# Kernel optimization log

Measured on AMD Instinct MI355X. Metric: run time of the kernel, lower is better.

The kernel has to match this reference:

```python
import jax, jax.numpy as jnp
import numpy as np

N = 50000
E = 1600000
IN_DIM = 64
EMB_DIM = 64
DENSE = 128
HEADS = 2
GATD = 64
SLOPE = 0.2


def gat_conv(x, src, dst, W, al, ar, b):
    # DGL GATConv: x [N, Fin], W [Fin, H*D], al/ar/b [H, D]
    n = x.shape[0]
    H, D = al.shape
    z = (x @ W).reshape(n, H, D)                      # [N,H,D]
    el = jnp.sum(z * al, axis=-1)                     # [N,H]
    er = jnp.sum(z * ar, axis=-1)                     # [N,H]
    e = jax.nn.leaky_relu(el[src] + er[dst], SLOPE)   # [E,H]
    # edge softmax grouped by destination node
    m = jax.ops.segment_max(e, dst, num_segments=n)   # [N,H]
    ex = jnp.exp(e - m[dst])                          # [E,H]
    s = jax.ops.segment_sum(ex, dst, num_segments=n)  # [N,H]
    alpha = ex / s[dst]                               # [E,H]
    out = jax.ops.segment_sum(alpha[:, :, None] * z[src], dst, num_segments=n)
    return out + b                                    # [N,H,D]


def setup_inputs() -> dict:
    key = jax.random.key(0)
    ks = jax.random.split(key, 20)
    g = lambda k, sh: jax.random.normal(k, sh, dtype=jnp.float32) * 0.05
    inp = {
        "feat": jax.random.normal(ks[0], (N, IN_DIM), dtype=jnp.float32),
        "node_ids": jax.random.randint(ks[1], (N,), 0, N, dtype=jnp.int32),
        "src": jax.random.randint(ks[2], (E,), 0, N, dtype=jnp.int32),
        "dst": jax.random.randint(ks[3], (E,), 0, N, dtype=jnp.int32),
        "emb": g(ks[4], (N, EMB_DIM)),
        "dense_w": g(ks[5], (IN_DIM + EMB_DIM, DENSE)),
        "dense_b": jnp.zeros((DENSE,), jnp.float32),
        "g1_w": g(ks[6], (DENSE, HEADS * GATD)),
        "g1_al": g(ks[7], (HEADS, GATD)),
        "g1_ar": g(ks[8], (HEADS, GATD)),
        "g1_b": jnp.zeros((HEADS, GATD), jnp.float32),
        "g2_w": g(ks[9], (HEADS * GATD, HEADS * GATD)),
        "g2_al": g(ks[10], (HEADS, GATD)),
        "g2_ar": g(ks[11], (HEADS, GATD)),
        "g2_b": jnp.zeros((HEADS, GATD), jnp.float32),
        "out_w": g(ks[12], (HEADS * GATD, 1)),
        "out_al": g(ks[13], (1, 1)),
        "out_ar": g(ks[14], (1, 1)),
        "out_b": jnp.zeros((1, 1), jnp.float32),
    }
    return inp


def reference(feat, node_ids, src, dst, emb, dense_w, dense_b,
              g1_w, g1_al, g1_ar, g1_b, g2_w, g2_al, g2_ar, g2_b,
              out_w, out_al, out_ar, out_b):
    # embedding concat + initial dense + ReLU
    h = jnp.concatenate([emb[node_ids], feat], axis=-1)   # [N, 128]
    h = jax.nn.relu(h @ dense_w + dense_b)                # [N, 128]
    # GAT layer 1: ReLU then concat heads (reshape N, H*D)
    h = jax.nn.relu(gat_conv(h, src, dst, g1_w, g1_al, g1_ar, g1_b))
    h = h.reshape(h.shape[0], -1)                         # [N, H*D]
    # GAT layer 2
    h = jax.nn.relu(gat_conv(h, src, dst, g2_w, g2_al, g2_ar, g2_b))
    h = h.reshape(h.shape[0], -1)
    # output GAT layer, 1 head, squeeze head dim
    h = gat_conv(h, src, dst, out_w, out_al, out_ar, out_b)  # [N,1,1]
    return h[:, 0, :]                                        # [N,1]
```

## Files before the change

### kernel.cpp

```cpp
#include <hip/hip_runtime.h>
#include <cfloat>
#include <cmath>


#define CBG 256
#define CAPC 12288
#define TILE 4096
#define BIMG 10240

typedef __attribute__((ext_vector_type(8))) short short8v;
typedef __attribute__((ext_vector_type(4))) float f32x4;

__device__ __forceinline__ float lrelu(float x) { return x > 0.f ? x : 0.2f * x; }

__device__ __forceinline__ uint32_t bf16_rne(float f) {
  uint32_t u = __float_as_uint(f);
  return (u + 0x7fffu + ((u >> 16) & 1u)) >> 16;
}
__device__ __forceinline__ uint32_t pack_hilo(float v) {
  uint32_t h = bf16_rne(v);
  float r = v - __uint_as_float(h << 16);
  return (h << 16) | bf16_rne(r);
}

__global__ __launch_bounds__(256) void bucketA_kernel(
    const int* __restrict__ src, const int* __restrict__ dst,
    int* __restrict__ scount, uint32_t* __restrict__ tmp, int e, int ncb) {
  __shared__ int cnt[256];
  __shared__ int lscan[256];
  __shared__ int gbase[256];
  __shared__ uint32_t image[TILE];
  const int t = threadIdx.x;
  const int e0 = blockIdx.x * TILE;
  const int ne = min(TILE, e - e0);

  for (int i = t; i < 256; i += 256) cnt[i] = 0;
  __syncthreads();
  for (int i = t; i < ne; i += 256) atomicAdd(&cnt[dst[e0 + i] >> 8], 1);
  __syncthreads();
  if (t < 64) {
    int carry = 0;
    for (int base = 0; base < ncb; base += 64) {
      int idx = base + t;
      int c = (idx < ncb) ? cnt[idx] : 0;
      int v = c;
#pragma unroll
      for (int off = 1; off < 64; off <<= 1) {
        int u = __shfl_up(v, off, 64);
        if (t >= off) v += u;
      }
      if (idx < ncb) lscan[idx] = carry + v - c;
      carry += __shfl(v, 63, 64);
    }
  }
  __syncthreads();
  for (int b = t; b < ncb; b += 256)
    gbase[b] = (cnt[b] > 0) ? atomicAdd(&scount[b], cnt[b]) : 0;
  __syncthreads();
  for (int b = t; b < ncb; b += 256) cnt[b] = 0;
  __syncthreads();
  for (int i = t; i < ne; i += 256) {
    int d = dst[e0 + i], s = src[e0 + i];
    int b = d >> 8;
    int r = atomicAdd(&cnt[b], 1);
    image[lscan[b] + r] =
        (uint32_t)s | ((uint32_t)(d & 255) << 16) | ((uint32_t)b << 24);
  }
  __syncthreads();
  for (int j = t; j < ne; j += 256) {
    uint32_t w = image[j];
    int b = w >> 24;
    int pos = gbase[b] + (j - lscan[b]);
    if (pos < CAPC) tmp[(size_t)b * CAPC + pos] = w & 0xFFFFFFu;
  }
}

__global__ __launch_bounds__(256) void bucketB_kernel(
    const uint32_t* __restrict__ tmp, const int* __restrict__ scount,
    int* __restrict__ row_start, int* __restrict__ csr_src, int n, int ncb, int e) {
  __shared__ int cnt[256];
  __shared__ int cur[256];
  __shared__ int wsum[4];
  __shared__ int s_base;
  __shared__ uint32_t image[BIMG];
  const int b = blockIdx.x, t = threadIdx.x, lane = t & 63, wid = t >> 6;

  if (t < 64) {
    int part = 0;
    for (int idx = lane; idx < b; idx += 64) part += scount[idx];
#pragma unroll
    for (int off = 32; off; off >>= 1) part += __shfl_xor(part, off, 64);
    if (lane == 0) s_base = part;
  }
  cnt[t] = 0;
  __syncthreads();
  const int total = min(scount[b], CAPC);
  const int base = s_base;
  const uint32_t* strm = tmp + (size_t)b * CAPC;

  for (int i = t; i < total; i += 256) atomicAdd(&cnt[(strm[i] >> 16) & 255], 1);
  __syncthreads();
  int c = cnt[t], v = c;
#pragma unroll
  for (int off = 1; off < 64; off <<= 1) {
    int u = __shfl_up(v, off, 64);
    if (lane >= off) v += u;
  }
  if (lane == 63) wsum[wid] = v;
  __syncthreads();
  if (t == 0) {
    int acc = 0;
#pragma unroll
    for (int w = 0; w < 4; w++) { int x = wsum[w]; wsum[w] = acc; acc += x; }
  }
  __syncthreads();
  int ex = wsum[wid] + v - c;
  cur[t] = ex;
  int d = b * CBG + t;
  if (d < n) row_start[d] = base + ex;
  if (b == 0 && t == 0) row_start[n] = e;
  __syncthreads();
  for (int i = t; i < total; i += 256) {
    uint32_t w = strm[i];
    int dl = (w >> 16) & 255;
    int pos = atomicAdd(&cur[dl], 1);
    if (pos < BIMG) image[pos] = w & 0xFFFFu;
    else csr_src[base + pos] = (int)(w & 0xFFFFu);
  }
  __syncthreads();
  const int lim = total < BIMG ? total : BIMG;
  for (int j = t; j < lim; j += 256) csr_src[base + j] = (int)image[j];
}

__global__ void hist_kernel(const int* __restrict__ dst, int* __restrict__ cnt, int e) {
  for (int i = blockIdx.x * blockDim.x + threadIdx.x; i < e; i += gridDim.x * blockDim.x)
    atomicAdd(&cnt[dst[i]], 1);
}
__global__ void scatter_kernel(const int* __restrict__ src, const int* __restrict__ dst,
                               const int* __restrict__ row_start, int* __restrict__ cursor,
                               int* __restrict__ csr_src, int e) {
  for (int i = blockIdx.x * blockDim.x + threadIdx.x; i < e; i += gridDim.x * blockDim.x) {
    int d = dst[i];
    int pos = atomicAdd(&cursor[d], 1);
    csr_src[row_start[d] + pos] = src[i];
  }
}
__global__ __launch_bounds__(1024) void scan1_kernel(const int* __restrict__ cnt,
                                                     int* __restrict__ row_start,
                                                     int* __restrict__ bsum, int n) {
  __shared__ int wsum[16];
  const int t = threadIdx.x, lane = t & 63, wid = t >> 6;
  int i = blockIdx.x * 1024 + t;
  int c = (i < n) ? cnt[i] : 0;
  int v = c;
#pragma unroll
  for (int off = 1; off < 64; off <<= 1) {
    int u = __shfl_up(v, off, 64);
    if (lane >= off) v += u;
  }
  if (lane == 63) wsum[wid] = v;
  __syncthreads();
  if (t == 0) {
    int acc = 0;
#pragma unroll
    for (int w = 0; w < 16; w++) { int x = wsum[w]; wsum[w] = acc; acc += x; }
    bsum[blockIdx.x] = acc;
  }
  __syncthreads();
  if (i < n) row_start[i] = wsum[wid] + v - c;
}
__global__ __launch_bounds__(64) void scan2_kernel(int* __restrict__ bsum, int nb) {
  const int lane = threadIdx.x;
  int carry = 0;
  for (int base = 0; base < nb; base += 64) {
    int idx = base + lane;
    int c = (idx < nb) ? bsum[idx] : 0;
    int v = c;
#pragma unroll
    for (int off = 1; off < 64; off <<= 1) {
      int u = __shfl_up(v, off, 64);
      if (lane >= off) v += u;
    }
    if (idx < nb) bsum[idx] = carry + v - c;
    carry += __shfl(v, 63, 64);
  }
}
__global__ void scan3_kernel(int* __restrict__ row_start, const int* __restrict__ bsum,
                             int n, int e) {
  int i = blockIdx.x * blockDim.x + threadIdx.x;
  if (i < n) row_start[i] += bsum[i >> 10];
  if (i == 0) row_start[n] = e;
}

__global__ __launch_bounds__(256) void wswz3_kernel(
    const float* __restrict__ W0, const float* __restrict__ W1,
    const float* __restrict__ W2, short* __restrict__ Whi0,
    short* __restrict__ Wlo0, short* __restrict__ Whi1, short* __restrict__ Wlo1,
    short* __restrict__ Whi2, short* __restrict__ Wlo2) {
  int which = blockIdx.x >> 3;
  const float* W = which == 0 ? W0 : (which == 1 ? W1 : W2);
  short* Whi = which == 0 ? Whi0 : (which == 1 ? Whi1 : Whi2);
  short* Wlo = which == 0 ? Wlo0 : (which == 1 ? Wlo1 : Wlo2);
  int fid = (blockIdx.x & 7) * 256 + threadIdx.x;
  int lane = fid & 63;
  int cq = fid >> 6;
  int q = cq >> 3, c = cq & 7;
  int col = c * 16 + (lane & 15);
  int k0 = q * 32 + (lane >> 4) * 8;
#pragma unroll
  for (int j = 0; j < 8; j++) {
    float v = W[(k0 + j) * 128 + col];
    uint32_t h = bf16_rne(v);
    float r = v - __uint_as_float(h << 16);
    Whi[fid * 8 + j] = (short)h;
    Wlo[fid * 8 + j] = (short)bf16_rne(r);
  }
}

template <int MODE>
__global__ __launch_bounds__(256) void mfmm_kernel(
    const uint32_t* __restrict__ Xp, const short* __restrict__ Whi,
    const short* __restrict__ Wlo, const float* __restrict__ bias,
    uint32_t* __restrict__ Hp, uint32_t* __restrict__ zp,
    float2* __restrict__ el2, float2* __restrict__ er2,
    const float* __restrict__ al, const float* __restrict__ ar, int n,
    const float* __restrict__ emb, const int* __restrict__ ids,
    const float* __restrict__ feat) {
  __shared__ short Ahi[64 * 136];
  __shared__ short Alo[64 * 136];
  const int t = threadIdx.x;
  const int nb = blockIdx.x * 64;

  for (int idx = t; idx < 64 * 32; idx += 256) {
    int nl = idx >> 5, k4 = (idx & 31) << 2;
    int node = nb + nl;
    uint32_t h01 = 0, h23 = 0, l01 = 0, l23 = 0;
    if (node < n) {
      if (MODE == 1) {
        uint4 w = *(const uint4*)&Xp[(size_t)node * 128 + k4];
        h01 = (w.x >> 16) | (w.y & 0xffff0000u);
        l01 = (w.x & 0xffffu) | (w.y << 16);
        h23 = (w.z >> 16) | (w.w & 0xffff0000u);
        l23 = (w.z & 0xffffu) | (w.w << 16);
      } else {
        float4 v;
        if (k4 < 64) v = *(const float4*)&emb[(size_t)ids[node] * 64 + k4];
        else         v = *(const float4*)&feat[(size_t)node * 64 + (k4 - 64)];
        uint32_t a0 = bf16_rne(v.x), a1 = bf16_rne(v.y);
        uint32_t a2 = bf16_rne(v.z), a3 = bf16_rne(v.w);
        h01 = a0 | (a1 << 16);
        h23 = a2 | (a3 << 16);
        l01 = bf16_rne(v.x - __uint_as_float(a0 << 16)) |
              (bf16_rne(v.y - __uint_as_float(a1 << 16)) << 16);
        l23 = bf16_rne(v.z - __uint_as_float(a2 << 16)) |
              (bf16_rne(v.w - __uint_as_float(a3 << 16)) << 16);
      }
    }
    *(uint2*)&Ahi[nl * 136 + k4] = make_uint2(h01, h23);
    *(uint2*)&Alo[nl * 136 + k4] = make_uint2(l01, l23);
  }
  __syncthreads();

  const int lane = t & 63, wv = t >> 6;
  const int r16 = lane & 15, g = lane >> 4;
  const int arow = (wv * 16 + r16) * 136;

  f32x4 acc[8];
#pragma unroll
  for (int c = 0; c < 8; c++) acc[c] = (f32x4){0.f, 0.f, 0.f, 0.f};

#pragma unroll
  for (int q = 0; q < 4; q++) {
    int ka = q * 32 + g * 8;
    short8v ahi = *(const short8v*)&Ahi[arow + ka];
    short8v alo = *(const short8v*)&Alo[arow + ka];
#pragma unroll
    for (int c = 0; c < 8; c++) {
      short8v bhi = *(const short8v*)&Whi[(((q * 8 + c) * 64) + lane) * 8];
      short8v blo = *(const short8v*)&Wlo[(((q * 8 + c) * 64) + lane) * 8];
      acc[c] = __builtin_amdgcn_mfma_f32_16x16x32_bf16(ahi, bhi, acc[c], 0, 0, 0);
      acc[c] = __builtin_amdgcn_mfma_f32_16x16x32_bf16(ahi, blo, acc[c], 0, 0, 0);
      acc[c] = __builtin_amdgcn_mfma_f32_16x16x32_bf16(alo, bhi, acc[c], 0, 0, 0);
    }
  }

  const int node_base = nb + wv * 16;
  if (MODE == 0) {
#pragma unroll
    for (int c = 0; c < 8; c++) {
      int col = c * 16 + r16;
      float bv = bias[col];
#pragma unroll
      for (int r = 0; r < 4; r++) {
        int node = node_base + g * 4 + r;
        if (node < n) {
          float v = fmaxf(acc[c][r] + bv, 0.f);
          Hp[(size_t)node * 128 + col] = pack_hilo(v);
        }
      }
    }
  } else {
    float p0l[4] = {0, 0, 0, 0}, p1l[4] = {0, 0, 0, 0};
    float p0r[4] = {0, 0, 0, 0}, p1r[4] = {0, 0, 0, 0};
#pragma unroll
    for (int c = 0; c < 8; c++) {
      int col = c * 16 + r16;
      float av = al[col], rv = ar[col];
#pragma unroll
      for (int r = 0; r < 4; r++) {
        if (c < 4) { p0l[r] = fmaf(acc[c][r], av, p0l[r]); p0r[r] = fmaf(acc[c][r], rv, p0r[r]); }
        else       { p1l[r] = fmaf(acc[c][r], av, p1l[r]); p1r[r] = fmaf(acc[c][r], rv, p1r[r]); }
      }
    }
#pragma unroll
    for (int c = 0; c < 8; c++) {
#pragma unroll
      for (int r = 0; r < 4; r++) {
        float other = __shfl_xor(acc[c][r], 1, 64);
        int node = node_base + g * 4 + r;
        if (!(lane & 1) && node < n) {
          uint32_t w = bf16_rne(acc[c][r]) | (bf16_rne(other) << 16);
          zp[(size_t)node * 64 + c * 8 + (r16 >> 1)] = w;
        }
      }
    }
#pragma unroll
    for (int off = 1; off < 16; off <<= 1) {
#pragma unroll
      for (int r = 0; r < 4; r++) {
        p0l[r] += __shfl_xor(p0l[r], off, 64);
        p1l[r] += __shfl_xor(p1l[r], off, 64);
        p0r[r] += __shfl_xor(p0r[r], off, 64);
        p1r[r] += __shfl_xor(p1r[r], off, 64);
      }
    }
    if (r16 == 0) {
#pragma unroll
      for (int r = 0; r < 4; r++) {
        int node = node_base + g * 4 + r;
        if (node < n) {
          el2[node] = make_float2(p0l[r], p1l[r]);
          er2[node] = make_float2(p0r[r], p1r[r]);
        }
      }
    }
  }
}

#define CAP 256
__global__ __launch_bounds__(256) void agg12_kernel(
    const uint32_t* __restrict__ zp, const float2* __restrict__ el2,
    const float2* __restrict__ er2, const int* __restrict__ row_start,
    const int* __restrict__ csr_src, const float* __restrict__ bias,
    uint32_t* __restrict__ Hp,
    const float* __restrict__ ow, const float* __restrict__ oal,
    const float* __restrict__ oar, float* __restrict__ z3,
    float* __restrict__ el3, float* __restrict__ er3, int n, int fuse_out) {
  __shared__ float2 ec[4][CAP];
  __shared__ int sc[4][CAP];
  const int w = threadIdx.x >> 6, lane = threadIdx.x & 63;
  const int node = blockIdx.x * 4 + w;
  const bool valid = node < n;
  int rs = 0, deg = 0;
  float er0 = 0.f, er1 = 0.f;
  if (valid) {
    rs = row_start[node];
    deg = row_start[node + 1] - rs;
    float2 e2 = er2[node];
    er0 = e2.x; er1 = e2.y;
  }
  const int cdeg = deg < CAP ? deg : CAP;

  float sp0 = 0.f, sp1 = 0.f;
  for (int i = lane; i < deg; i += 64) {
    int s = csr_src[rs + i];
    float2 l = el2[s];
    float x0 = __expf(lrelu(l.x + er0));
    float x1 = __expf(lrelu(l.y + er1));
    if (i < CAP) { sc[w][i] = s; ec[w][i] = make_float2(x0, x1); }
    sp0 += x0; sp1 += x1;
  }
#pragma unroll
  for (int off = 32; off; off >>= 1) {
    sp0 += __shfl_xor(sp0, off, 64);
    sp1 += __shfl_xor(sp1, off, 64);
  }
  __syncthreads();

  float ae = 0.f, ao = 0.f;
  int i = 0;
  for (; i + 8 <= cdeg; i += 8) {
    uint32_t zw[8];
    float xh[8];
#pragma unroll
    for (int u = 0; u < 8; u++) {
      int s = sc[w][i + u];
      float2 ex = ec[w][i + u];
      xh[u] = (lane < 32) ? ex.x : ex.y;
      zw[u] = zp[(size_t)s * 64 + lane];
    }
#pragma unroll
    for (int u = 0; u < 8; u++) {
      ae = fmaf(xh[u], __uint_as_float(zw[u] << 16), ae);
      ao = fmaf(xh[u], __uint_as_float(zw[u] & 0xffff0000u), ao);
    }
  }
  for (; i < cdeg; i++) {
    int s = sc[w][i];
    float2 ex = ec[w][i];
    float x = (lane < 32) ? ex.x : ex.y;
    uint32_t zw = zp[(size_t)s * 64 + lane];
    ae = fmaf(x, __uint_as_float(zw << 16), ae);
    ao = fmaf(x, __uint_as_float(zw & 0xffff0000u), ao);
  }
  for (; i < deg; i++) {
    int s = csr_src[rs + i];
    float2 l = el2[s];
    float x0 = __expf(lrelu(l.x + er0));
    float x1 = __expf(lrelu(l.y + er1));
    float x = (lane < 32) ? x0 : x1;
    uint32_t zw = zp[(size_t)s * 64 + lane];
    ae = fmaf(x, __uint_as_float(zw << 16), ae);
    ao = fmaf(x, __uint_as_float(zw & 0xffff0000u), ao);
  }

  if (valid) {
    float sp = (lane < 32) ? sp0 : sp1;
    float2 b2 = reinterpret_cast<const float2*>(bias)[lane];
    float oe, oo;
    if (deg == 0) { oe = b2.x; oo = b2.y; }
    else { oe = ae / sp + b2.x; oo = ao / sp + b2.y; }
    oe = fmaxf(oe, 0.f);
    oo = fmaxf(oo, 0.f);
    if (!fuse_out) {
      *(uint2*)&Hp[(size_t)node * 128 + 2 * lane] =
          make_uint2(pack_hilo(oe), pack_hilo(oo));
    } else {
      float2 w2 = reinterpret_cast<const float2*>(ow)[lane];
      float d = oe * w2.x + oo * w2.y;
#pragma unroll
      for (int off = 32; off; off >>= 1) d += __shfl_xor(d, off, 64);
      if (lane == 0) {
        z3[node] = d;
        el3[node] = d * oal[0];
        er3[node] = d * oar[0];
      }
    }
  }
}

__global__ __launch_bounds__(256) void agg3_kernel(
    const float* __restrict__ z3, const float* __restrict__ el3,
    const float* __restrict__ er3, const int* __restrict__ row_start,
    const int* __restrict__ csr_src, const float* __restrict__ b,
    float* __restrict__ out, int n) {
  int node = blockIdx.x * 8 + (threadIdx.x >> 5);
  int l32 = threadIdx.x & 31;
  if (node >= n) return;
  int rs = row_start[node];
  int deg = row_start[node + 1] - rs;
  float er = er3[node];
  float sp = 0.f, ap = 0.f;
  for (int i = l32; i < deg; i += 32) {
    int s = csr_src[rs + i];
    float ex = __expf(lrelu(el3[s] + er));
    sp += ex;
    ap = fmaf(ex, z3[s], ap);
  }
#pragma unroll
  for (int off = 16; off; off >>= 1) {
    sp += __shfl_xor(sp, off, 64);
    ap += __shfl_xor(ap, off, 64);
  }
  if (l32 == 0) out[node] = (deg == 0) ? b[0] : (ap / sp + b[0]);
}

extern "C" void kernel_launch(void* const* d_in, const int* in_sizes, int n_in,
                              void* d_out, int out_size, void* d_ws, size_t ws_size,
                              hipStream_t stream) {
  const float* feat     = (const float*)d_in[0];
  const int*   node_ids = (const int*)d_in[1];
  const int*   src      = (const int*)d_in[2];
  const int*   dst      = (const int*)d_in[3];
  const float* emb      = (const float*)d_in[4];
  const float* dense_w  = (const float*)d_in[5];
  const float* dense_b  = (const float*)d_in[6];
  const float* g1_w     = (const float*)d_in[7];
  const float* g1_al    = (const float*)d_in[8];
  const float* g1_ar    = (const float*)d_in[9];
  const float* g1_b     = (const float*)d_in[10];
  const float* g2_w     = (const float*)d_in[11];
  const float* g2_al    = (const float*)d_in[12];
  const float* g2_ar    = (const float*)d_in[13];
  const float* g2_b     = (const float*)d_in[14];
  const float* out_w    = (const float*)d_in[15];
  const float* out_al   = (const float*)d_in[16];
  const float* out_ar   = (const float*)d_in[17];
  const float* out_b    = (const float*)d_in[18];
  const int n = in_sizes[0] / 64;
  const int e = in_sizes[2];

  const int ncb = (n + CBG - 1) / CBG;

  char* ws = (char*)d_ws;
  size_t off = 0;
  auto alloc = [&](size_t bytes) -> void* {
    void* p = ws + off;
    off += (bytes + 255) & ~(size_t)255;
    return p;
  };
  uint32_t* Hp       = (uint32_t*)alloc((size_t)n * 128 * 4);
  size_t zp_bytes    = (size_t)n * 64 * 4;
  size_t tmp_bytes   = (size_t)ncb * CAPC * 4;
  uint32_t* zp       = (uint32_t*)alloc(zp_bytes > tmp_bytes ? zp_bytes : tmp_bytes);
  uint32_t* tmp      = zp;
  float2*   el2      = (float2*)alloc((size_t)n * 8);
  float2*   er2      = (float2*)alloc((size_t)n * 8);
  float*    z3       = (float*)alloc((size_t)n * 4);
  float*    el3      = (float*)alloc((size_t)n * 4);
  float*    er3      = (float*)alloc((size_t)n * 4);
  int*      scount   = (int*)alloc((size_t)ncb * 4);
  int*      row_start= (int*)alloc((size_t)(n + 1) * 4);
  int*      csr_src  = (int*)alloc((size_t)e * 4);
  short*    Wd_hi    = (short*)alloc(2048 * 8 * 2);
  short*    Wd_lo    = (short*)alloc(2048 * 8 * 2);
  short*    W1_hi    = (short*)alloc(2048 * 8 * 2);
  short*    W1_lo    = (short*)alloc(2048 * 8 * 2);
  short*    W2_hi    = (short*)alloc(2048 * 8 * 2);
  short*    W2_lo    = (short*)alloc(2048 * 8 * 2);
  int*      cnt      = (int*)alloc((size_t)n * 4);
  int*      cursor   = (int*)alloc((size_t)n * 4);
  const int nblk     = (n + 1023) / 1024;
  int*      bsum     = (int*)alloc((size_t)nblk * 4);

  wswz3_kernel<<<24, 256, 0, stream>>>(dense_w, g1_w, g2_w,
                                       Wd_hi, Wd_lo, W1_hi, W1_lo, W2_hi, W2_lo);

  if (n < 65536) {
    hipMemsetAsync(scount, 0, (size_t)ncb * 4, stream);
    const int natile = (e + TILE - 1) / TILE;
    bucketA_kernel<<<natile, 256, 0, stream>>>(src, dst, scount, tmp, e, ncb);
    bucketB_kernel<<<ncb, 256, 0, stream>>>(tmp, scount, row_start, csr_src,
                                            n, ncb, e);
  } else {
    hipMemsetAsync(cnt, 0, (size_t)n * 4, stream);
    hipMemsetAsync(cursor, 0, (size_t)n * 4, stream);
    hist_kernel<<<2048, 256, 0, stream>>>(dst, cnt, e);
    scan1_kernel<<<nblk, 1024, 0, stream>>>(cnt, row_start, bsum, n);
    scan2_kernel<<<1, 64, 0, stream>>>(bsum, nblk);
    scan3_kernel<<<(n + 255) / 256, 256, 0, stream>>>(row_start, bsum, n, e);
    scatter_kernel<<<2048, 256, 0, stream>>>(src, dst, row_start, cursor, csr_src, e);
  }

  const int mmgrid = (n + 63) / 64;
  const int ngrid4 = (n + 3) / 4;
  const int ngrid8 = (n + 7) / 8;

  mfmm_kernel<0><<<mmgrid, 256, 0, stream>>>(nullptr, Wd_hi, Wd_lo, dense_b,
                                             Hp, nullptr, nullptr, nullptr,
                                             nullptr, nullptr, n, emb, node_ids, feat);
  mfmm_kernel<1><<<mmgrid, 256, 0, stream>>>(Hp, W1_hi, W1_lo, nullptr,
                                             nullptr, zp, el2, er2,
                                             g1_al, g1_ar, n, nullptr, nullptr, nullptr);
  agg12_kernel<<<ngrid4, 256, 0, stream>>>(zp, el2, er2, row_start, csr_src, g1_b, Hp,
                                           nullptr, nullptr, nullptr, nullptr, nullptr,
                                           nullptr, n, 0);
  mfmm_kernel<1><<<mmgrid, 256, 0, stream>>>(Hp, W2_hi, W2_lo, nullptr,
                                             nullptr, zp, el2, er2,
                                             g2_al, g2_ar, n, nullptr, nullptr, nullptr);
  agg12_kernel<<<ngrid4, 256, 0, stream>>>(zp, el2, er2, row_start, csr_src, g2_b, nullptr,
                                           out_w, out_al, out_ar, z3, el3, er3, n, 1);
  agg3_kernel<<<ngrid8, 256, 0, stream>>>(z3, el3, er3, row_start, csr_src, out_b,
                                          (float*)d_out, n);
}
```

Before: 240.3 us.

## Fuse CSR bucket pass with dense layer; fold memset into weight prep

Replaces the scount memset with an extra block in the weight-swizzle kernel, and merges bucketB with the first dense matmul into one launch whose blocks split by index. The two stages are independent, so they can run concurrently and the launch count drops. Bucket tile size is halved to give bucketA more blocks. The shared memory buffer is now sized for the larger of the two bodies, which may lower occupancy for the matmul blocks.

```diff
diff --git a/kernel.cpp b/kernel.cpp
--- a/kernel.cpp
+++ b/kernel.cpp
@@ -5,7 +5,7 @@
 
 #define CBG 256
 #define CAPC 12288
-#define TILE 4096
+#define TILE 2048
 #define BIMG 10240
 
 typedef __attribute__((ext_vector_type(8))) short short8v;
@@ -21,6 +21,36 @@
   uint32_t h = bf16_rne(v);
   float r = v - __uint_as_float(h << 16);
   return (h << 16) | bf16_rne(r);
+}
+
+__global__ __launch_bounds__(256) void prep_kernel(
+    const float* __restrict__ W0, const float* __restrict__ W1,
+    const float* __restrict__ W2, short* __restrict__ Whi0,
+    short* __restrict__ Wlo0, short* __restrict__ Whi1, short* __restrict__ Wlo1,
+    short* __restrict__ Whi2, short* __restrict__ Wlo2,
+    int* __restrict__ scount, int ncb) {
+  if (blockIdx.x >= 24) {
+    for (int i = threadIdx.x; i < ncb; i += 256) scount[i] = 0;
+    return;
+  }
+  int which = blockIdx.x >> 3;
+  const float* W = which == 0 ? W0 : (which == 1 ? W1 : W2);
+  short* Whi = which == 0 ? Whi0 : (which == 1 ? Whi1 : Whi2);
+  short* Wlo = which == 0 ? Wlo0 : (which == 1 ? Wlo1 : Wlo2);
+  int fid = (blockIdx.x & 7) * 256 + threadIdx.x;
+  int lane = fid & 63;
+  int cq = fid >> 6;
+  int q = cq >> 3, c = cq & 7;
+  int col = c * 16 + (lane & 15);
+  int k0 = q * 32 + (lane >> 4) * 8;
+#pragma unroll
+  for (int j = 0; j < 8; j++) {
+    float v = W[(k0 + j) * 128 + col];
+    uint32_t h = bf16_rne(v);
+    float r = v - __uint_as_float(h << 16);
+    Whi[fid * 8 + j] = (short)h;
+    Wlo[fid * 8 + j] = (short)bf16_rne(r);
+  }
 }
 
 __global__ __launch_bounds__(256) void bucketA_kernel(
@@ -75,27 +105,28 @@
   }
 }
 
-__global__ __launch_bounds__(256) void bucketB_kernel(
-    const uint32_t* __restrict__ tmp, const int* __restrict__ scount,
-    int* __restrict__ row_start, int* __restrict__ csr_src, int n, int ncb, int e) {
-  __shared__ int cnt[256];
-  __shared__ int cur[256];
-  __shared__ int wsum[4];
-  __shared__ int s_base;
-  __shared__ uint32_t image[BIMG];
-  const int b = blockIdx.x, t = threadIdx.x, lane = t & 63, wid = t >> 6;
+__device__ __forceinline__ void bucketB_body(
+    int b, char* smem, const uint32_t* __restrict__ tmp,
+    const int* __restrict__ scount, int* __restrict__ row_start,
+    int* __restrict__ csr_src, int n, int ncb, int e) {
+  int* cnt = (int*)smem;
+  int* cur = cnt + 256;
+  int* wsum = cur + 256;
+  int* s_base = wsum + 4;
+  uint32_t* image = (uint32_t*)(smem + 2080);
+  const int t = threadIdx.x, lane = t & 63, wid = t >> 6;
 
   if (t < 64) {
     int part = 0;
     for (int idx = lane; idx < b; idx += 64) part += scount[idx];
 #pragma unroll
     for (int off = 32; off; off >>= 1) part += __shfl_xor(part, off, 64);
-    if (lane == 0) s_base = part;
+    if (lane == 0) *s_base = part;
   }
   cnt[t] = 0;
   __syncthreads();
   const int total = min(scount[b], CAPC);
-  const int base = s_base;
+  const int base = *s_base;
   const uint32_t* strm = tmp + (size_t)b * CAPC;
 
   for (int i = t; i < total; i += 256) atomicAdd(&cnt[(strm[i] >> 16) & 255], 1);
@@ -132,93 +163,9 @@
   for (int j = t; j < lim; j += 256) csr_src[base + j] = (int)image[j];
 }
 
-__global__ void hist_kernel(const int* __restrict__ dst, int* __restrict__ cnt, int e) {
-  for (int i = blockIdx.x * blockDim.x + threadIdx.x; i < e; i += gridDim.x * blockDim.x)
-    atomicAdd(&cnt[dst[i]], 1);
-}
-__global__ void scatter_kernel(const int* __restrict__ src, const int* __restrict__ dst,
-                               const int* __restrict__ row_start, int* __restrict__ cursor,
-                               int* __restrict__ csr_src, int e) {
-  for (int i = blockIdx.x * blockDim.x + threadIdx.x; i < e; i += gridDim.x * blockDim.x) {
-    int d = dst[i];
-    int pos = atomicAdd(&cursor[d], 1);
-    csr_src[row_start[d] + pos] = src[i];
-  }
-}
-__global__ __launch_bounds__(1024) void scan1_kernel(const int* __restrict__ cnt,
-                                                     int* __restrict__ row_start,
-                                                     int* __restrict__ bsum, int n) {
-  __shared__ int wsum[16];
-  const int t = threadIdx.x, lane = t & 63, wid = t >> 6;
-  int i = blockIdx.x * 1024 + t;
-  int c = (i < n) ? cnt[i] : 0;
-  int v = c;
-#pragma unroll
-  for (int off = 1; off < 64; off <<= 1) {
-    int u = __shfl_up(v, off, 64);
-    if (lane >= off) v += u;
-  }
-  if (lane == 63) wsum[wid] = v;
-  __syncthreads();
-  if (t == 0) {
-    int acc = 0;
-#pragma unroll
-    for (int w = 0; w < 16; w++) { int x = wsum[w]; wsum[w] = acc; acc += x; }
-    bsum[blockIdx.x] = acc;
-  }
-  __syncthreads();
-  if (i < n) row_start[i] = wsum[wid] + v - c;
-}
-__global__ __launch_bounds__(64) void scan2_kernel(int* __restrict__ bsum, int nb) {
-  const int lane = threadIdx.x;
-  int carry = 0;
-  for (int base = 0; base < nb; base += 64) {
-    int idx = base + lane;
-    int c = (idx < nb) ? bsum[idx] : 0;
-    int v = c;
-#pragma unroll
-    for (int off = 1; off < 64; off <<= 1) {
-      int u = __shfl_up(v, off, 64);
-      if (lane >= off) v += u;
-    }
-    if (idx < nb) bsum[idx] = carry + v - c;
-    carry += __shfl(v, 63, 64);
-  }
-}
-__global__ void scan3_kernel(int* __restrict__ row_start, const int* __restrict__ bsum,
-                             int n, int e) {
-  int i = blockIdx.x * blockDim.x + threadIdx.x;
-  if (i < n) row_start[i] += bsum[i >> 10];
-  if (i == 0) row_start[n] = e;
-}
-
-__global__ __launch_bounds__(256) void wswz3_kernel(
-    const float* __restrict__ W0, const float* __restrict__ W1,
-    const float* __restrict__ W2, short* __restrict__ Whi0,
-    short* __restrict__ Wlo0, short* __restrict__ Whi1, short* __restrict__ Wlo1,
-    short* __restrict__ Whi2, short* __restrict__ Wlo2) {
-  int which = blockIdx.x >> 3;
-  const float* W = which == 0 ? W0 : (which == 1 ? W1 : W2);
-  short* Whi = which == 0 ? Whi0 : (which == 1 ? Whi1 : Whi2);
-  short* Wlo = which == 0 ? Wlo0 : (which == 1 ? Wlo1 : Wlo2);
-  int fid = (blockIdx.x & 7) * 256 + threadIdx.x;
-  int lane = fid & 63;
-  int cq = fid >> 6;
-  int q = cq >> 3, c = cq & 7;
-  int col = c * 16 + (lane & 15);
-  int k0 = q * 32 + (lane >> 4) * 8;
-#pragma unroll
-  for (int j = 0; j < 8; j++) {
-    float v = W[(k0 + j) * 128 + col];
-    uint32_t h = bf16_rne(v);
-    float r = v - __uint_as_float(h << 16);
-    Whi[fid * 8 + j] = (short)h;
-    Wlo[fid * 8 + j] = (short)bf16_rne(r);
-  }
-}
-
 template <int MODE>
-__global__ __launch_bounds__(256) void mfmm_kernel(
+__device__ __forceinline__ void mfmm_body(
+    int bid, char* smem,
     const uint32_t* __restrict__ Xp, const short* __restrict__ Whi,
     const short* __restrict__ Wlo, const float* __restrict__ bias,
     uint32_t* __restrict__ Hp, uint32_t* __restrict__ zp,
@@ -226,10 +173,10 @@
     const float* __restrict__ al, const float* __restrict__ ar, int n,
     const float* __restrict__ emb, const int* __restrict__ ids,
     const float* __restrict__ feat) {
-  __shared__ short Ahi[64 * 136];
-  __shared__ short Alo[64 * 136];
+  short* Ahi = (short*)smem;
+  short* Alo = Ahi + 64 * 136;
   const int t = threadIdx.x;
-  const int nb = blockIdx.x * 64;
+  const int nb = bid * 64;
 
   for (int idx = t; idx < 64 * 32; idx += 256) {
     int nl = idx >> 5, k4 = (idx & 31) << 2;
@@ -345,6 +292,92 @@
       }
     }
   }
+}
+
+__global__ __launch_bounds__(256) void mfmm0_bktB_kernel(
+    const uint32_t* __restrict__ tmp, const int* __restrict__ scount,
+    int* __restrict__ row_start, int* __restrict__ csr_src, int ncbB,
+    const short* __restrict__ Whi, const short* __restrict__ Wlo,
+    const float* __restrict__ bias, uint32_t* __restrict__ Hp, int n, int ncb,
+    int e, const float* __restrict__ emb, const int* __restrict__ ids,
+    const float* __restrict__ feat) {
+  __shared__ __align__(16) char smem[43040];
+  if ((int)blockIdx.x < ncbB) {
+    bucketB_body(blockIdx.x, smem, tmp, scount, row_start, csr_src, n, ncb, e);
+  } else {
+    mfmm_body<0>(blockIdx.x - ncbB, smem, nullptr, Whi, Wlo, bias, Hp,
+                 nullptr, nullptr, nullptr, nullptr, nullptr, n, emb, ids, feat);
+  }
+}
+
+__global__ __launch_bounds__(256) void mfmm1_kernel(
+    const uint32_t* __restrict__ Xp, const short* __restrict__ Whi,
+    const short* __restrict__ Wlo, uint32_t* __restrict__ zp,
+    float2* __restrict__ el2, float2* __restrict__ er2,
+    const float* __restrict__ al, const float* __restrict__ ar, int n) {
+  __shared__ __align__(16) char smem[64 * 136 * 2 * 2];
+  mfmm_body<1>(blockIdx.x, smem, Xp, Whi, Wlo, nullptr, nullptr, zp, el2, er2,
+               al, ar, n, nullptr, nullptr, nullptr);
+}
+
+__global__ void hist_kernel(const int* __restrict__ dst, int* __restrict__ cnt, int e) {
+  for (int i = blockIdx.x * blockDim.x + threadIdx.x; i < e; i += gridDim.x * blockDim.x)
+    atomicAdd(&cnt[dst[i]], 1);
+}
+__global__ void scatter_kernel(const int* __restrict__ src, const int* __restrict__ dst,
+                               const int* __restrict__ row_start, int* __restrict__ cursor,
+                               int* __restrict__ csr_src, int e) {
+  for (int i = blockIdx.x * blockDim.x + threadIdx.x; i < e; i += gridDim.x * blockDim.x) {
+    int d = dst[i];
+    int pos = atomicAdd(&cursor[d], 1);
+    csr_src[row_start[d] + pos] = src[i];
+  }
+}
+__global__ __launch_bounds__(1024) void scan1_kernel(const int* __restrict__ cnt,
+                                                     int* __restrict__ row_start,
+                                                     int* __restrict__ bsum, int n) {
+  __shared__ int wsum[16];
+  const int t = threadIdx.x, lane = t & 63, wid = t >> 6;
+  int i = blockIdx.x * 1024 + t;
+  int c = (i < n) ? cnt[i] : 0;
+  int v = c;
+#pragma unroll
+  for (int off = 1; off < 64; off <<= 1) {
+    int u = __shfl_up(v, off, 64);
+    if (lane >= off) v += u;
+  }
+  if (lane == 63) wsum[wid] = v;
+  __syncthreads();
+  if (t == 0) {
+    int acc = 0;
+#pragma unroll
+    for (int w = 0; w < 16; w++) { int x = wsum[w]; wsum[w] = acc; acc += x; }
+    bsum[blockIdx.x] = acc;
+  }
+  __syncthreads();
+  if (i < n) row_start[i] = wsum[wid] + v - c;
+}
+__global__ __launch_bounds__(64) void scan2_kernel(int* __restrict__ bsum, int nb) {
+  const int lane = threadIdx.x;
+  int carry = 0;
+  for (int base = 0; base < nb; base += 64) {
+    int idx = base + lane;
+    int c = (idx < nb) ? bsum[idx] : 0;
+    int v = c;
+#pragma unroll
+    for (int off = 1; off < 64; off <<= 1) {
+      int u = __shfl_up(v, off, 64);
+      if (lane >= off) v += u;
+    }
+    if (idx < nb) bsum[idx] = carry + v - c;
+    carry += __shfl(v, 63, 64);
+  }
+}
+__global__ void scan3_kernel(int* __restrict__ row_start, const int* __restrict__ bsum,
+                             int n, int e) {
+  int i = blockIdx.x * blockDim.x + threadIdx.x;
+  if (i < n) row_start[i] += bsum[i >> 10];
+  if (i == 0) row_start[n] = e;
 }
 
 #define CAP 256
@@ -533,15 +566,20 @@
   const int nblk     = (n + 1023) / 1024;
   int*      bsum     = (int*)alloc((size_t)nblk * 4);
 
-  wswz3_kernel<<<24, 256, 0, stream>>>(dense_w, g1_w, g2_w,
-                                       Wd_hi, Wd_lo, W1_hi, W1_lo, W2_hi, W2_lo);
+  const int mmgrid = (n + 63) / 64;
+  const int ngrid4 = (n + 3) / 4;
+  const int ngrid8 = (n + 7) / 8;
+
+  prep_kernel<<<25, 256, 0, stream>>>(dense_w, g1_w, g2_w,
+                                      Wd_hi, Wd_lo, W1_hi, W1_lo, W2_hi, W2_lo,
+                                      scount, ncb);
 
   if (n < 65536) {
-    hipMemsetAsync(scount, 0, (size_t)ncb * 4, stream);
     const int natile = (e + TILE - 1) / TILE;
     bucketA_kernel<<<natile, 256, 0, stream>>>(src, dst, scount, tmp, e, ncb);
-    bucketB_kernel<<<ncb, 256, 0, stream>>>(tmp, scount, row_start, csr_src,
-                                            n, ncb, e);
+    mfmm0_bktB_kernel<<<ncb + mmgrid, 256, 0, stream>>>(
+        tmp, scount, row_start, csr_src, ncb,
+        Wd_hi, Wd_lo, dense_b, Hp, n, ncb, e, emb, node_ids, feat);
   } else {
     hipMemsetAsync(cnt, 0, (size_t)n * 4, stream);
     hipMemsetAsync(cursor, 0, (size_t)n * 4, stream);
@@ -550,24 +588,18 @@
     scan2_kernel<<<1, 64, 0, stream>>>(bsum, nblk);
     scan3_kernel<<<(n + 255) / 256, 256, 0, stream>>>(row_start, bsum, n, e);
     scatter_kernel<<<2048, 256, 0, stream>>>(src, dst, row_start, cursor, csr_src, e);
-  }
-
-  const int mmgrid = (n + 63) / 64;
-  const int ngrid4 = (n + 3) / 4;
-  const int ngrid8 = (n + 7) / 8;
-
-  mfmm_kernel<0><<<mmgrid, 256, 0, stream>>>(nullptr, Wd_hi, Wd_lo, dense_b,
-                                             Hp, nullptr, nullptr, nullptr,
-                                             nullptr, nullptr, n, emb, node_ids, feat);
-  mfmm_kernel<1><<<mmgrid, 256, 0, stream>>>(Hp, W1_hi, W1_lo, nullptr,
-                                             nullptr, zp, el2, er2,
-                                             g1_al, g1_ar, n, nullptr, nullptr, nullptr);
+    mfmm0_bktB_kernel<<<mmgrid, 256, 0, stream>>>(
+        tmp, scount, row_start, csr_src, 0,
+        Wd_hi, Wd_lo, dense_b, Hp, n, ncb, e, emb, node_ids, feat);
+  }
+
+  mfmm1_kernel<<<mmgrid, 256, 0, stream>>>(Hp, W1_hi, W1_lo, zp, el2, er2,
+                                           g1_al, g1_ar, n);
   agg12_kernel<<<ngrid4, 256, 0, stream>>>(zp, el2, er2, row_start, csr_src, g1_b, Hp,
                                            nullptr, nullptr, nullptr, nullptr, nullptr,
                                            nullptr, n, 0);
-  mfmm_kernel<1><<<mmgrid, 256, 0, stream>>>(Hp, W2_hi, W2_lo, nullptr,
-                                             nullptr, zp, el2, er2,
-                                             g2_al, g2_ar, n, nullptr, nullptr, nullptr);
+  mfmm1_kernel<<<mmgrid, 256, 0, stream>>>(Hp, W2_hi, W2_lo, zp, el2, er2,
+                                           g2_al, g2_ar, n);
   agg12_kernel<<<ngrid4, 256, 0, stream>>>(zp, el2, er2, row_start, csr_src, g2_b, nullptr,
                                            out_w, out_al, out_ar, z3, el3, er3, n, 1);
   agg3_kernel<<<ngrid8, 256, 0, stream>>>(z3, el3, er3, row_start, csr_src, out_b,
```

Result: no change. 237.8 us (-1.1%).
